# Optimization experiments

Measured on AMD Instinct MI355X. Metric: run time of the kernel, lower is better.

## Reference

```python
import jax, jax.numpy as jnp
import numpy as np
from jax import lax

ITERATIONS = 8
KT, KH, KW = 3, 7, 7


def _ssm_op(left, right):
    a1, b1 = left
    a2, b2 = right
    return (a1 * a2, a2 * b1 + b2)


def setup_inputs() -> dict:
    key = jax.random.key(0)
    k1, k2, k3 = jax.random.split(key, 3)
    B, T, H, W, C = 1, 16, 64, 64, 128
    x = jax.random.normal(k1, (B, T, H, W, C), dtype=jnp.float32)
    A_kernel = 0.02 * jax.random.normal(k2, (C, KT, KH, KW), dtype=jnp.float32)
    B_kernel = 0.02 * jax.random.normal(k3, (C, KT, KH, KW), dtype=jnp.float32)
    return {"x": x, "A_kernel": A_kernel, "B_kernel": B_kernel}


def _pad_kernel_fft(kern, T, H, W):
    # Place (C, kt, kh, kw) kernel circularly centered into a (C, T, H, W) canvas, FFT it.
    C = kern.shape[0]
    t_idx = (jnp.arange(KT) - KT // 2) % T
    h_idx = (jnp.arange(KH) - KH // 2) % H
    w_idx = (jnp.arange(KW) - KW // 2) % W
    tt, th, tw = jnp.meshgrid(t_idx, h_idx, w_idx, indexing="ij")
    padded = jnp.zeros((C, T, H, W), dtype=kern.dtype).at[:, tt, th, tw].set(kern)
    kf = jnp.fft.fftn(padded, axes=(1, 2, 3))  # (C, T, H, W) complex
    return kf.transpose(1, 2, 3, 0)[None, ...]  # (1, T, H, W, C)


def reference(x, A_kernel, B_kernel):
    B, T, H, W, C = x.shape
    A_stable = 0.9 * jnp.tanh(A_kernel)
    A_f = _pad_kernel_fft(A_stable, T, H, W)   # (1,T,H,W,C)
    B_f = _pad_kernel_fft(B_kernel, T, H, W)   # (1,T,H,W,C)
    x_f = jnp.fft.fftn(x, axes=(1, 2, 3))      # (B,T,H,W,C)
    Bx_f = B_f * x_f
    a_seq = jnp.broadcast_to(A_f, (ITERATIONS, B, T, H, W, C))
    b_seq = jnp.broadcast_to(Bx_f, (ITERATIONS, B, T, H, W, C))
    _, h_all_f = lax.associative_scan(_ssm_op, (a_seq, b_seq), axis=0)
    h_final = jnp.fft.ifftn(h_all_f[-1], axes=(1, 2, 3)).real
    return h_final
```

## Files before the change

kernel.cpp:

```cpp
#include <hip/hip_runtime.h>
#include <hip/hip_fp16.h>
#include <math.h>

#define TT 16
#define HH 64
#define WW 64
#define CC 128
#define PI2 6.283185307179586f

#define LROW(r) (((r) & 0x38) | ((((r) >> 3) ^ (r)) & 7))

__device__ __forceinline__ float2 cadd(float2 a, float2 b){ return make_float2(a.x+b.x, a.y+b.y); }
__device__ __forceinline__ float2 csub(float2 a, float2 b){ return make_float2(a.x-b.x, a.y-b.y); }
__device__ __forceinline__ float2 cmul(float2 a, float2 b) {
    return make_float2(a.x*b.x - a.y*b.y, a.x*b.y + a.y*b.x);
}
__device__ __forceinline__ float2 cmac(float2 acc, float2 a, float2 b) {
    acc.x = fmaf(a.x, b.x, fmaf(-a.y, b.y, acc.x));
    acc.y = fmaf(a.x, b.y, fmaf(a.y, b.x, acc.y));
    return acc;
}
__device__ __forceinline__ float2 csq(float2 a) {
    return make_float2(a.x*a.x - a.y*a.y, 2.f*a.x*a.y);
}

template<int SGN>
__device__ __forceinline__ void dft4(float2 b0, float2 b1, float2 b2, float2 b3,
                                     float2& y0, float2& y1, float2& y2, float2& y3) {
    float2 e0 = cadd(b0, b2), e1 = csub(b0, b2);
    float2 o0 = cadd(b1, b3), o1 = csub(b1, b3);
    y0 = cadd(e0, o0); y2 = csub(e0, o0);
    float2 r = make_float2((float)(-SGN) * o1.y, (float)SGN * o1.x);
    y1 = cadd(e1, r); y3 = csub(e1, r);
}

template<int SGN>
__device__ __forceinline__ void dft8(const float2* a, float2* X) {
    const float C = 0.70710678118654752f;
    float2 E0,E1,E2,E3,O0,O1,O2,O3;
    dft4<SGN>(a[0],a[2],a[4],a[6], E0,E1,E2,E3);
    dft4<SGN>(a[1],a[3],a[5],a[7], O0,O1,O2,O3);
    float2 T1 = make_float2(C*(O1.x - (float)SGN*O1.y), C*((float)SGN*O1.x + O1.y));
    float2 T2 = make_float2((float)(-SGN)*O2.y, (float)SGN*O2.x);
    float2 T3 = make_float2(-C*(O3.x + (float)SGN*O3.y), C*((float)SGN*O3.x - O3.y));
    X[0]=cadd(E0,O0); X[4]=csub(E0,O0);
    X[1]=cadd(E1,T1); X[5]=csub(E1,T1);
    X[2]=cadd(E2,T2); X[6]=csub(E2,T2);
    X[3]=cadd(E3,T3); X[7]=csub(E3,T3);
}

template<int SGN>
__device__ __forceinline__ void dft16(const float2* v, float2* X) {
    const float ct[10] = {1.f, 0.92387953251f, 0.70710678119f, 0.38268343236f, 0.f,
                          0.f, -0.70710678119f, 0.f, 0.f, -0.92387953251f};
    const float st[10] = {0.f, 0.38268343236f, 0.70710678119f, 0.92387953251f, 1.f,
                          0.f, 0.70710678119f, 0.f, 0.f, -0.38268343236f};
    float2 Z[16];
    #pragma unroll
    for (int h0 = 0; h0 < 4; ++h0) {
        float2 y0,y1,y2,y3;
        dft4<SGN>(v[h0], v[4+h0], v[8+h0], v[12+h0], y0,y1,y2,y3);
        float2 ys[4] = {y0,y1,y2,y3};
        #pragma unroll
        for (int k0 = 0; k0 < 4; ++k0) {
            int m = h0 * k0;
            float cc = ct[m], ss = (float)SGN * st[m];
            Z[k0*4 + h0] = make_float2(ys[k0].x*cc - ys[k0].y*ss,
                                       ys[k0].x*ss + ys[k0].y*cc);
        }
    }
    #pragma unroll
    for (int k0 = 0; k0 < 4; ++k0) {
        float2 y0,y1,y2,y3;
        dft4<SGN>(Z[k0*4+0], Z[k0*4+1], Z[k0*4+2], Z[k0*4+3], y0,y1,y2,y3);
        X[k0] = y0; X[k0+4] = y1; X[k0+8] = y2; X[k0+12] = y3;
    }
}


__global__ __launch_bounds__(256) void pA(const float* __restrict__ x,
                                          uint4* __restrict__ Z,
                                          const float* __restrict__ Ak,
                                          const float* __restrict__ Bk,
                                          __half2* __restrict__ Ahw,
                                          __half2* __restrict__ Bhw) {
    __shared__ __align__(16) char smem[49664];
    int bid = blockIdx.x;
    int tid = threadIdx.x;
    if (bid < 1024) {
        __half2 (*zs)[64][32] = (__half2(*)[64][32])smem;
        __half2 (*sp)[33][32] = (__half2(*)[33][32])(smem + 32768);
        int cq = bid & 3, hq = (bid >> 2) & 15, t = bid >> 6;
        int c = tid & 31, s4 = tid >> 5;
        float twc[8], tws[8];
        {
            float s1, c1; sincosf(-PI2 * s4 / 64.0f, &s1, &c1);
            twc[0] = 1.f; tws[0] = 0.f;
            #pragma unroll
            for (int k = 1; k < 8; ++k) {
                twc[k] = twc[k-1]*c1 - tws[k-1]*s1;
                tws[k] = twc[k-1]*s1 + tws[k-1]*c1;
            }
        }
        const float* xb = x + (size_t)(t*64 + hq*4) * 8192 + cq * 32 + c;
        float xr[4][8];
        #pragma unroll
        for (int hh = 0; hh < 4; ++hh)
            #pragma unroll
            for (int h1 = 0; h1 < 8; ++h1)
                xr[hh][h1] = xb[(size_t)hh * 8192 + (h1*8 + s4) * 128];
        #pragma unroll
        for (int hh = 0; hh < 4; ++hh) {
            float2 a[8], Y[8];
            #pragma unroll
            for (int h1 = 0; h1 < 8; ++h1) a[h1] = make_float2(xr[hh][h1], 0.f);
            dft8<-1>(a, Y);
            #pragma unroll
            for (int k0 = 0; k0 < 8; ++k0) {
                float2 z = make_float2(Y[k0].x*twc[k0] - Y[k0].y*tws[k0],
                                       Y[k0].x*tws[k0] + Y[k0].y*twc[k0]);
                zs[hh][k0*8 + s4][c] = __float22half2_rn(z);
            }
        }
        __syncthreads();
        #pragma unroll
        for (int hh = 0; hh < 4; ++hh) {
            float2 b[8], X[8];
            #pragma unroll
            for (int h0 = 0; h0 < 8; ++h0)
                b[h0] = __half22float2(zs[hh][s4*8 + h0][c]);
            dft8<-1>(b, X);
            #pragma unroll
            for (int k1 = 0; k1 < 8; ++k1) {
                int om = s4 + 8 * k1;
                if (om <= 32) sp[hh][om][c] = __float22half2_rn(X[k1]);
            }
        }
        __syncthreads();
        for (int i = tid; i < 1056; i += 256) {
            int hh = i & 3, ccl = (i >> 2) & 7, om = i >> 5;
            uint4 u = *(const uint4*)&sp[hh][om][ccl * 4];
            Z[(((size_t)(om*32 + cq*8 + ccl)*16 + t)*64 + hq*4 + hh)] = u;
        }
    } else {
        float (*Asl)[7][64] = (float(*)[7][64])smem;
        float (*Bsl)[7][64] = (float(*)[7][64])(smem + 12544);
        float2 (*Awl)[64]   = (float2(*)[64])(smem + 25088);
        float2 (*Bwl)[64]   = (float2(*)[64])(smem + 28672);
        float2* tw64        = (float2*)(smem + 32256);
        int kid = bid - 1024;
        int kt = kid / 66;
        int rem = kid % 66;
        int om = rem >> 1, chalf = rem & 1;
        int c0 = chalf * 64;
        for (int i = tid; i < 64; i += 256) {
            float s, cw; sincosf(-PI2 * i / 64.0f, &s, &cw);
            tw64[i] = make_float2(cw, s);
        }
        for (int i = tid; i < 49 * 64; i += 256) {
            int p = i >> 6, cl = i & 63;
            int kh = p / 7, kw = p % 7;
            int idx = (((c0 + cl) * 3 + kt) * 7 + kh) * 7 + kw;
            Asl[kh][kw][cl] = 0.9f * tanhf(Ak[idx]);
            Bsl[kh][kw][cl] = Bk[idx];
        }
        __syncthreads();
        for (int i = tid; i < 7 * 64; i += 256) {
            int kh = i >> 6, cl = i & 63;
            float2 aA = make_float2(0.f,0.f), aB = make_float2(0.f,0.f);
            #pragma unroll
            for (int kw = 0; kw < 7; ++kw) {
                float2 tw = tw64[(om * (kw - 3)) & 63];
                float va = Asl[kh][kw][cl], vb = Bsl[kh][kw][cl];
                aA.x = fmaf(va, tw.x, aA.x); aA.y = fmaf(va, tw.y, aA.y);
                aB.x = fmaf(vb, tw.x, aB.x); aB.y = fmaf(vb, tw.y, aB.y);
            }
            Awl[kh][cl] = aA; Bwl[kh][cl] = aB;
        }
        __syncthreads();
        for (int i = tid; i < 64 * 64; i += 256) {
            int eta = i >> 6, cl = i & 63;
            float2 aA = make_float2(0.f,0.f), aB = make_float2(0.f,0.f);
            #pragma unroll
            for (int kh = 0; kh < 7; ++kh) {
                float2 tw = tw64[(eta * (kh - 3)) & 63];
                aA = cmac(aA, Awl[kh][cl], tw);
                aB = cmac(aB, Bwl[kh][cl], tw);
            }
            int ep = ((eta & 7) << 3) | (eta >> 3);
            int o = ((kt * 33 + om) * 64 + ep) * 128 + c0 + cl;
            Ahw[o] = __float22half2_rn(aA);
            Bhw[o] = __float22half2_rn(aB);
        }
    }
}

__global__ __launch_bounds__(256) void pmid(uint4* __restrict__ Z,
                                            const __half2* __restrict__ Ahw,
                                            const __half2* __restrict__ Bhw) {
    __shared__ __half2 tl[16][64][4];
    int l = (blockIdx.x & 7) * 132 + (blockIdx.x >> 3);
    int om = l >> 5, cc = l & 31;
    int c0 = cc * 4;
    int tid = threadIdx.x;
    uint4* g = Z + (size_t)l * 1024;

    int d = tid & 7;
    float twc[8], tws[8];
    {
        float s1, c1; sincosf(-PI2 * d / 64.0f, &s1, &c1);
        twc[0] = 1.f; tws[0] = 0.f;
        #pragma unroll
        for (int k = 1; k < 8; ++k) {
            twc[k] = twc[k-1]*c1 - tws[k-1]*s1;
            tws[k] = twc[k-1]*s1 + tws[k-1]*c1;
        }
    }
    for (int i = tid; i < 1024; i += 256) {
        uint4 u = g[i];
        int t = i >> 6, h = i & 63;
        int pr = LROW(h);
        tl[t][pr][0] = *(__half2*)&u.x;
        tl[t][pr][1] = *(__half2*)&u.y;
        tl[t][pr][2] = *(__half2*)&u.z;
        tl[t][pr][3] = *(__half2*)&u.w;
    }
    __syncthreads();
    int cl = (tid >> 3) & 3, ts = tid >> 5;
    #pragma unroll
    for (int q = 0; q < 2; ++q) {
        int t = ts*2 + q;
        float2 a[8], Y[8];
        #pragma unroll
        for (int h1 = 0; h1 < 8; ++h1)
            a[h1] = __half22float2(tl[t][LROW(h1*8 + d)][cl]);
        dft8<-1>(a, Y);
        #pragma unroll
        for (int k0 = 0; k0 < 8; ++k0) {
            float2 z = make_float2(Y[k0].x*twc[k0] - Y[k0].y*tws[k0],
                                   Y[k0].x*tws[k0] + Y[k0].y*twc[k0]);
            tl[t][LROW(k0*8 + d)][cl] = __float22half2_rn(z);
        }
    }
    __syncthreads();
    #pragma unroll
    for (int q = 0; q < 2; ++q) {
        int t = ts*2 + q;
        float2 a[8], Y[8];
        #pragma unroll
        for (int h0 = 0; h0 < 8; ++h0)
            a[h0] = __half22float2(tl[t][LROW(d*8 + h0)][cl]);
        dft8<-1>(a, Y);
        #pragma unroll
        for (int k1 = 0; k1 < 8; ++k1)
            tl[t][LROW(d*8 + k1)][cl] = __float22half2_rn(Y[k1]);
    }
    __syncthreads();
    {
        const float CT16[16] = {1.f, 0.9238795325f, 0.7071067812f, 0.3826834324f, 0.f,
                                -0.3826834324f, -0.7071067812f, -0.9238795325f, -1.f,
                                -0.9238795325f, -0.7071067812f, -0.3826834324f, 0.f,
                                0.3826834324f, 0.7071067812f, 0.9238795325f};
        const float ST16[16] = {0.f, 0.3826834324f, 0.7071067812f, 0.9238795325f, 1.f,
                                0.9238795325f, 0.7071067812f, 0.3826834324f, 0.f,
                                -0.3826834324f, -0.7071067812f, -0.9238795325f, -1.f,
                                -0.9238795325f, -0.7071067812f, -0.3826834324f};
        int cg = tid & 3, rT = tid >> 2;
        const int PKT = 33 * 64 * 128;
        int kb = (om * 64 + rT) * 128 + c0 + cg;
        float2 A0 = __half22float2(Ahw[kb]);
        float2 A1 = __half22float2(Ahw[kb + PKT]);
        float2 A2 = __half22float2(Ahw[kb + 2*PKT]);
        float2 B0 = __half22float2(Bhw[kb]);
        float2 B1 = __half22float2(Bhw[kb + PKT]);
        float2 B2 = __half22float2(Bhw[kb + 2*PKT]);
        int pr = LROW(rT);
        float2 v[16], X[16];
        #pragma unroll
        for (int t = 0; t < 16; ++t) v[t] = __half22float2(tl[t][pr][cg]);
        dft16<-1>(v, X);
        #pragma unroll
        for (int ta = 0; ta < 16; ++ta) {
            float2 wv = make_float2(CT16[ta], -ST16[ta]);
            float2 wc = make_float2(CT16[ta],  ST16[ta]);
            float2 Af = A1; Af = cmac(Af, A0, wc); Af = cmac(Af, A2, wv);
            float2 Bf = B1; Bf = cmac(Bf, B0, wc); Bf = cmac(Bf, B2, wv);
            float2 A2q = csq(Af), A4q = csq(A2q);
            float2 S = cmul(make_float2(1.f+Af.x, Af.y), make_float2(1.f+A2q.x, A2q.y));
            S = cmul(S, make_float2(1.f+A4q.x, A4q.y));
            float2 G = cmul(S, Bf);
            X[ta] = cmul(X[ta], G);
        }
        dft16<1>(X, v);
        const float sc = 0.015625f;
        #pragma unroll
        for (int t = 0; t < 16; ++t)
            tl[t][pr][cg] = __float22half2_rn(make_float2(v[t].x*sc, v[t].y*sc));
    }
    __syncthreads();
    #pragma unroll
    for (int q = 0; q < 2; ++q) {
        int t = ts*2 + q;
        float2 a[8], Y[8];
        #pragma unroll
        for (int e1 = 0; e1 < 8; ++e1)
            a[e1] = __half22float2(tl[t][LROW(d*8 + e1)][cl]);
        dft8<1>(a, Y);
        #pragma unroll
        for (int h0 = 0; h0 < 8; ++h0) {
            float2 z = make_float2( Y[h0].x*twc[h0] + Y[h0].y*tws[h0],
                                   -Y[h0].x*tws[h0] + Y[h0].y*twc[h0]);
            tl[t][LROW(d*8 + h0)][cl] = __float22half2_rn(z);
        }
    }
    __syncthreads();
    #pragma unroll
    for (int q = 0; q < 2; ++q) {
        int t = ts*2 + q;
        float2 a[8], Y[8];
        #pragma unroll
        for (int e0 = 0; e0 < 8; ++e0)
            a[e0] = __half22float2(tl[t][LROW(e0*8 + d)][cl]);
        dft8<1>(a, Y);
        #pragma unroll
        for (int h1 = 0; h1 < 8; ++h1)
            tl[t][LROW(d + 8*h1)][cl] = __float22half2_rn(Y[h1]);
    }
    __syncthreads();
    for (int i = tid; i < 1024; i += 256) {
        int t = i >> 6, h = i & 63;
        int pr = LROW(h);
        uint4 u;
        __half2 v0 = tl[t][pr][0], v1 = tl[t][pr][1];
        __half2 v2 = tl[t][pr][2], v3 = tl[t][pr][3];
        u.x = *(unsigned int*)&v0; u.y = *(unsigned int*)&v1;
        u.z = *(unsigned int*)&v2; u.w = *(unsigned int*)&v3;
        g[i] = u;
    }
}

__global__ __launch_bounds__(256) void p5(const uint4* __restrict__ Z,
                                          float* __restrict__ out) {
    __shared__ __half2 plane[4][64][32];
    __shared__ float2 tw64[64];
    int bid = blockIdx.x;
    int cq = bid & 3, hq = (bid >> 2) & 15, t = bid >> 6;
    int tid = threadIdx.x;
    if (tid < 64) {
        float s, cw; sincosf(PI2 * tid / 64.0f, &s, &cw);
        tw64[tid] = make_float2(cw, s);
    }
    for (int i = tid; i < 1056; i += 256) {
        int hh = i & 3, ccl = (i >> 2) & 7, om = i >> 5;
        uint4 u = Z[(((size_t)(om*32 + cq*8 + ccl)*16 + t)*64 + hq*4 + hh)];
        *(uint4*)&plane[hh][om][ccl * 4] = u;
        if (om >= 1 && om <= 31) {
            __half2 m0 = *(__half2*)&u.x; m0.y = __hneg(m0.y);
            __half2 m1 = *(__half2*)&u.y; m1.y = __hneg(m1.y);
            __half2 m2 = *(__half2*)&u.z; m2.y = __hneg(m2.y);
            __half2 m3 = *(__half2*)&u.w; m3.y = __hneg(m3.y);
            plane[hh][64-om][ccl*4+0] = m0;
            plane[hh][64-om][ccl*4+1] = m1;
            plane[hh][64-om][ccl*4+2] = m2;
            plane[hh][64-om][ccl*4+3] = m3;
        }
    }
    __syncthreads();
    int c = tid & 31, s4 = tid >> 5;
    __half2 arh[4][8];
    #pragma unroll
    for (int hh = 0; hh < 4; ++hh)
        #pragma unroll
        for (int h1 = 0; h1 < 8; ++h1)
            arh[hh][h1] = plane[hh][h1*8 + s4][c];
    __syncthreads();
    #pragma unroll
    for (int hh = 0; hh < 4; ++hh) {
        float2 a[8], Y[8];
        #pragma unroll
        for (int h1 = 0; h1 < 8; ++h1) a[h1] = __half22float2(arh[hh][h1]);
        dft8<1>(a, Y);
        #pragma unroll
        for (int k0 = 0; k0 < 8; ++k0) {
            float2 z = cmul(Y[k0], tw64[(s4 * k0) & 63]);
            plane[hh][k0*8 + s4][c] = __float22half2_rn(z);
        }
    }
    __syncthreads();
    #pragma unroll
    for (int hh = 0; hh < 4; ++hh) {
        float2 b[8], X[8];
        #pragma unroll
        for (int h0 = 0; h0 < 8; ++h0)
            b[h0] = __half22float2(plane[hh][s4*8 + h0][c]);
        dft8<1>(b, X);
        float* dst = out + (size_t)(t*64 + hq*4 + hh) * 64 * 128 + cq * 32 + c;
        #pragma unroll
        for (int k1 = 0; k1 < 8; ++k1)
            dst[(size_t)(s4 + 8*k1) * 128] = X[k1].x * (1.0f / 1024.0f);
    }
}

extern "C" void kernel_launch(void* const* d_in, const int* in_sizes, int n_in,
                              void* d_out, int out_size, void* d_ws, size_t ws_size,
                              hipStream_t stream) {
    const float* x  = (const float*)d_in[0];
    const float* Ak = (const float*)d_in[1];
    const float* Bk = (const float*)d_in[2];
    float* out = (float*)d_out;

    uint4* Z = (uint4*)d_ws;
    __half2* Ahw = (__half2*)((char*)d_ws + (size_t)33*32*1024*16);
    __half2* Bhw = Ahw + 3 * 33 * 64 * 128;

    hipLaunchKernelGGL(pA,   dim3(1222), dim3(256), 0, stream, x, Z, Ak, Bk, Ahw, Bhw);
    hipLaunchKernelGGL(pmid, dim3(1056), dim3(256), 0, stream, Z, Ahw, Bhw);
    hipLaunchKernelGGL(p5,   dim3(1024), dim3(256), 0, stream, Z, out);
}
```

Before: 63.84 us.

## Pack two real rows into one complex FFT in forward and inverse passes

The forward 2D FFT now packs two real h-rows as the real and imaginary parts of one complex signal. It runs half as many dft8 passes and splits the two spectra afterwards using Hermitian symmetry. The inverse pass does the reverse: it combines two half-spectra into one complex transform and writes the real and imaginary outputs as two rows. This halves the FFT arithmetic and shared memory use in pA and p5, at the cost of extra split and combine work and a little more fp16 rounding.

```diff
diff --git a/kernel.cpp b/kernel.cpp
--- a/kernel.cpp
+++ b/kernel.cpp
@@ -84,12 +84,12 @@
                                           const float* __restrict__ Bk,
                                           __half2* __restrict__ Ahw,
                                           __half2* __restrict__ Bhw) {
-    __shared__ __align__(16) char smem[49664];
+    __shared__ __align__(16) char smem[32768];
     int bid = blockIdx.x;
     int tid = threadIdx.x;
     if (bid < 1024) {
-        __half2 (*zs)[64][32] = (__half2(*)[64][32])smem;
-        __half2 (*sp)[33][32] = (__half2(*)[33][32])(smem + 32768);
+        __half2 (*zs)[64][32]  = (__half2(*)[64][32])smem;
+        __half2 (*sp2)[64][32] = (__half2(*)[64][32])(smem + 16384);
         int cq = bid & 3, hq = (bid >> 2) & 15, t = bid >> 6;
         int c = tid & 31, s4 = tid >> 5;
         float twc[8], tws[8];
@@ -103,44 +103,60 @@
             }
         }
         const float* xb = x + (size_t)(t*64 + hq*4) * 8192 + cq * 32 + c;
-        float xr[4][8];
-        #pragma unroll
-        for (int hh = 0; hh < 4; ++hh)
-            #pragma unroll
-            for (int h1 = 0; h1 < 8; ++h1)
-                xr[hh][h1] = xb[(size_t)hh * 8192 + (h1*8 + s4) * 128];
-        #pragma unroll
-        for (int hh = 0; hh < 4; ++hh) {
+        #pragma unroll
+        for (int p = 0; p < 2; ++p) {
             float2 a[8], Y[8];
             #pragma unroll
-            for (int h1 = 0; h1 < 8; ++h1) a[h1] = make_float2(xr[hh][h1], 0.f);
+            for (int h1 = 0; h1 < 8; ++h1) {
+                size_t off = (size_t)(h1*8 + s4) * 128;
+                a[h1] = make_float2(xb[(size_t)(2*p) * 8192 + off],
+                                    xb[(size_t)(2*p+1) * 8192 + off]);
+            }
             dft8<-1>(a, Y);
             #pragma unroll
             for (int k0 = 0; k0 < 8; ++k0) {
                 float2 z = make_float2(Y[k0].x*twc[k0] - Y[k0].y*tws[k0],
                                        Y[k0].x*tws[k0] + Y[k0].y*twc[k0]);
-                zs[hh][k0*8 + s4][c] = __float22half2_rn(z);
+                zs[p][k0*8 + s4][c] = __float22half2_rn(z);
             }
         }
         __syncthreads();
         #pragma unroll
-        for (int hh = 0; hh < 4; ++hh) {
+        for (int p = 0; p < 2; ++p) {
             float2 b[8], X[8];
             #pragma unroll
             for (int h0 = 0; h0 < 8; ++h0)
-                b[h0] = __half22float2(zs[hh][s4*8 + h0][c]);
+                b[h0] = __half22float2(zs[p][s4*8 + h0][c]);
             dft8<-1>(b, X);
             #pragma unroll
-            for (int k1 = 0; k1 < 8; ++k1) {
-                int om = s4 + 8 * k1;
-                if (om <= 32) sp[hh][om][c] = __float22half2_rn(X[k1]);
-            }
+            for (int k1 = 0; k1 < 8; ++k1)
+                sp2[p][s4 + 8*k1][c] = __float22half2_rn(X[k1]);
         }
         __syncthreads();
-        for (int i = tid; i < 1056; i += 256) {
-            int hh = i & 3, ccl = (i >> 2) & 7, om = i >> 5;
-            uint4 u = *(const uint4*)&sp[hh][om][ccl * 4];
-            Z[(((size_t)(om*32 + cq*8 + ccl)*16 + t)*64 + hq*4 + hh)] = u;
+        for (int i = tid; i < 528; i += 256) {
+            int p = i & 1, ccl = (i >> 1) & 7, om = i >> 4;
+            int mo = (64 - om) & 63;
+            uint4 ua = *(const uint4*)&sp2[p][om][ccl * 4];
+            uint4 ub = *(const uint4*)&sp2[p][mo][ccl * 4];
+            uint4 u1, u2;
+            const unsigned int* pa = &ua.x;
+            const unsigned int* pb = &ub.x;
+            unsigned int* p1o = &u1.x;
+            unsigned int* p2o = &u2.x;
+            #pragma unroll
+            for (int j = 0; j < 4; ++j) {
+                float2 za = __half22float2(*(const __half2*)&pa[j]);
+                float2 zb = __half22float2(*(const __half2*)&pb[j]);
+                float2 X1 = make_float2(0.5f*(za.x + zb.x), 0.5f*(za.y - zb.y));
+                float2 X2 = make_float2(0.5f*(za.y + zb.y), 0.5f*(zb.x - za.x));
+                __half2 h1v = __float22half2_rn(X1);
+                __half2 h2v = __float22half2_rn(X2);
+                p1o[j] = *(unsigned int*)&h1v;
+                p2o[j] = *(unsigned int*)&h2v;
+            }
+            size_t base = ((size_t)(om*32 + cq*8 + ccl)*16 + t)*64 + hq*4;
+            Z[base + 2*p]     = u1;
+            Z[base + 2*p + 1] = u2;
         }
     } else {
         float (*Asl)[7][64] = (float(*)[7][64])smem;
@@ -341,7 +357,7 @@
 
 __global__ __launch_bounds__(256) void p5(const uint4* __restrict__ Z,
                                           float* __restrict__ out) {
-    __shared__ __half2 plane[4][64][32];
+    __shared__ __half2 pl[2][64][32];
     __shared__ float2 tw64[64];
     int bid = blockIdx.x;
     int cq = bid & 3, hq = (bid >> 2) & 15, t = bid >> 6;
@@ -350,54 +366,60 @@
         float s, cw; sincosf(PI2 * tid / 64.0f, &s, &cw);
         tw64[tid] = make_float2(cw, s);
     }
-    for (int i = tid; i < 1056; i += 256) {
-        int hh = i & 3, ccl = (i >> 2) & 7, om = i >> 5;
-        uint4 u = Z[(((size_t)(om*32 + cq*8 + ccl)*16 + t)*64 + hq*4 + hh)];
-        *(uint4*)&plane[hh][om][ccl * 4] = u;
-        if (om >= 1 && om <= 31) {
-            __half2 m0 = *(__half2*)&u.x; m0.y = __hneg(m0.y);
-            __half2 m1 = *(__half2*)&u.y; m1.y = __hneg(m1.y);
-            __half2 m2 = *(__half2*)&u.z; m2.y = __hneg(m2.y);
-            __half2 m3 = *(__half2*)&u.w; m3.y = __hneg(m3.y);
-            plane[hh][64-om][ccl*4+0] = m0;
-            plane[hh][64-om][ccl*4+1] = m1;
-            plane[hh][64-om][ccl*4+2] = m2;
-            plane[hh][64-om][ccl*4+3] = m3;
+    for (int i = tid; i < 528; i += 256) {
+        int p = i & 1, ccl = (i >> 1) & 7, om = i >> 4;
+        size_t base = ((size_t)(om*32 + cq*8 + ccl)*16 + t)*64 + hq*4;
+        uint4 ua = Z[base + 2*p];
+        uint4 ub = Z[base + 2*p + 1];
+        const unsigned int* pa = &ua.x;
+        const unsigned int* pb = &ub.x;
+        #pragma unroll
+        for (int j = 0; j < 4; ++j) {
+            float2 za = __half22float2(*(const __half2*)&pa[j]);
+            float2 zb = __half22float2(*(const __half2*)&pb[j]);
+            pl[p][om][ccl*4+j] = __float22half2_rn(make_float2(za.x - zb.y, za.y + zb.x));
+            if (om >= 1 && om <= 31) {
+                pl[p][64-om][ccl*4+j] =
+                    __float22half2_rn(make_float2(za.x + zb.y, zb.x - za.y));
+            }
         }
     }
     __syncthreads();
     int c = tid & 31, s4 = tid >> 5;
-    __half2 arh[4][8];
-    #pragma unroll
-    for (int hh = 0; hh < 4; ++hh)
+    __half2 arh[2][8];
+    #pragma unroll
+    for (int p = 0; p < 2; ++p)
         #pragma unroll
         for (int h1 = 0; h1 < 8; ++h1)
-            arh[hh][h1] = plane[hh][h1*8 + s4][c];
-    __syncthreads();
-    #pragma unroll
-    for (int hh = 0; hh < 4; ++hh) {
+            arh[p][h1] = pl[p][h1*8 + s4][c];
+    __syncthreads();
+    #pragma unroll
+    for (int p = 0; p < 2; ++p) {
         float2 a[8], Y[8];
         #pragma unroll
-        for (int h1 = 0; h1 < 8; ++h1) a[h1] = __half22float2(arh[hh][h1]);
+        for (int h1 = 0; h1 < 8; ++h1) a[h1] = __half22float2(arh[p][h1]);
         dft8<1>(a, Y);
         #pragma unroll
         for (int k0 = 0; k0 < 8; ++k0) {
             float2 z = cmul(Y[k0], tw64[(s4 * k0) & 63]);
-            plane[hh][k0*8 + s4][c] = __float22half2_rn(z);
-        }
-    }
-    __syncthreads();
-    #pragma unroll
-    for (int hh = 0; hh < 4; ++hh) {
+            pl[p][k0*8 + s4][c] = __float22half2_rn(z);
+        }
+    }
+    __syncthreads();
+    #pragma unroll
+    for (int p = 0; p < 2; ++p) {
         float2 b[8], X[8];
         #pragma unroll
         for (int h0 = 0; h0 < 8; ++h0)
-            b[h0] = __half22float2(plane[hh][s4*8 + h0][c]);
+            b[h0] = __half22float2(pl[p][s4*8 + h0][c]);
         dft8<1>(b, X);
-        float* dst = out + (size_t)(t*64 + hq*4 + hh) * 64 * 128 + cq * 32 + c;
-        #pragma unroll
-        for (int k1 = 0; k1 < 8; ++k1)
-            dst[(size_t)(s4 + 8*k1) * 128] = X[k1].x * (1.0f / 1024.0f);
+        float* dst = out + (size_t)(t*64 + hq*4 + 2*p) * 8192 + cq * 32 + c;
+        #pragma unroll
+        for (int k1 = 0; k1 < 8; ++k1) {
+            size_t o = (size_t)(s4 + 8*k1) * 128;
+            dst[o]        = X[k1].x * (1.0f / 1024.0f);
+            dst[o + 8192] = X[k1].y * (1.0f / 1024.0f);
+        }
     }
 }
 
```

Result: faster. 60.81 us (-4.7%).
